# Kernel optimization log

Hardware: AMD Instinct MI355X
Metric: run time of the kernel (lower is better)

The kernel has to match this reference:

```python
import jax, jax.numpy as jnp
import numpy as np

B, C, H, W = 16, 512, 48, 48


def setup_inputs() -> dict:
    key = jax.random.key(0)
    k1, k2 = jax.random.split(key)
    rgb = jax.random.normal(k1, (B, C, H, W), dtype=jnp.float32)
    depth = jax.random.normal(k2, (B, C, H, W), dtype=jnp.float32)
    return {"rgb": rgb, "depth": depth}


def reference(rgb, depth):
    b, c, h, w = rgb.shape
    hw = h * w
    q = rgb.reshape(b, c, hw)              # [B, C, HW]
    k = depth.reshape(b, c, hw)            # [B, C, HW]
    # channel-affinity: energy[b, i, j] = <rgb_chan_i, depth_chan_j>
    energy = jnp.einsum('bcn,bdn->bcd', q, k)   # [B, C, C]
    cl_index = jnp.argmax(energy, axis=2)       # [B, C] best-matching depth channel per rgb channel
    # gather matched depth channels and fuse
    gathered = depth[jnp.arange(b)[:, None], cl_index]  # [B, C, H, W]
    return rgb + gathered
```

## Files before the change

kernel.cpp:

```cpp
#include <hip/hip_runtime.h>
#include <stdint.h>

#define BATCH 16
#define CH    512
#define HW    2304

typedef _Float16 half8  __attribute__((ext_vector_type(8)));
typedef float    f32x16 __attribute__((ext_vector_type(16)));

#define MFMA16 __builtin_amdgcn_mfma_f32_32x32x16_f16

#define DELTA 3.5f

#define ENERGY_ELEMS ((size_t)BATCH * CH * CH)
#define KSP     4
#define WS_NEED (KSP * ENERGY_ELEMS * 4)

#define LGKM_BARRIER() do { \
    asm volatile("s_waitcnt lgkmcnt(0)" ::: "memory"); \
    __builtin_amdgcn_s_barrier(); \
    __builtin_amdgcn_sched_barrier(0); \
} while (0)

__device__ __forceinline__ uint32_t f32_sortable(float f) {
    uint32_t u = __float_as_uint(f);
    return (u & 0x80000000u) ? ~u : (u | 0x80000000u);
}

__device__ __forceinline__ int swzs(int r, int s) {
    return r * 128 + ((s ^ ((r >> 1) & 7)) << 4);
}

__device__ __forceinline__ half8 cvt8h(const float4& v0, const float4& v1) {
    half8 h;
    h[0] = (_Float16)v0.x; h[1] = (_Float16)v0.y;
    h[2] = (_Float16)v0.z; h[3] = (_Float16)v0.w;
    h[4] = (_Float16)v1.x; h[5] = (_Float16)v1.y;
    h[6] = (_Float16)v1.z; h[7] = (_Float16)v1.w;
    return h;
}

#define BK3   64
#define KRANGE (HW / KSP)
#define NST   (KRANGE / BK3)
#define A3_OFF 0
#define B3_OFF 32768
#define BUF3_SZ 65536

__device__ __forceinline__ void load_tile3(const float* aT, const float* bT,
                                           float4 (&av)[8], float4 (&bv)[8]) {
    #pragma unroll
    for (int i = 0; i < 8; ++i) av[i] = *(const float4*)(aT + 4 * i);
    #pragma unroll
    for (int i = 0; i < 8; ++i) bv[i] = *(const float4*)(bT + 4 * i);
}

__device__ __forceinline__ void stage_tile3(char* dst,
                                            const float4 (&av)[8], const float4 (&bv)[8],
                                            int arow, int ah) {
    #pragma unroll
    for (int j = 0; j < 4; ++j)
        *(half8*)(dst + A3_OFF + swzs(arow, 4 * ah + j)) = cvt8h(av[2 * j], av[2 * j + 1]);
    #pragma unroll
    for (int j = 0; j < 4; ++j)
        *(half8*)(dst + B3_OFF + swzs(arow, 4 * ah + j)) = cvt8h(bv[2 * j], bv[2 * j + 1]);
}

__device__ __forceinline__ void compute_tile3(const char* buf, int rA0, int rB0, int hf,
                                              f32x16 (&acc)[2][4]) {
    __builtin_amdgcn_s_setprio(1);
    #pragma unroll
    for (int kc = 0; kc < 4; ++kc) {
        const int s0 = 2 * kc + hf;
        half8 a0 = *(const half8*)(buf + A3_OFF + swzs(rA0,      s0));
        half8 a1 = *(const half8*)(buf + A3_OFF + swzs(rA0 + 32, s0));
        half8 b0 = *(const half8*)(buf + B3_OFF + swzs(rB0,      s0));
        half8 b1 = *(const half8*)(buf + B3_OFF + swzs(rB0 + 32, s0));
        half8 b2 = *(const half8*)(buf + B3_OFF + swzs(rB0 + 64, s0));
        half8 b3 = *(const half8*)(buf + B3_OFF + swzs(rB0 + 96, s0));
        acc[0][0] = MFMA16(a0, b0, acc[0][0], 0, 0, 0);
        acc[0][1] = MFMA16(a0, b1, acc[0][1], 0, 0, 0);
        acc[0][2] = MFMA16(a0, b2, acc[0][2], 0, 0, 0);
        acc[0][3] = MFMA16(a0, b3, acc[0][3], 0, 0, 0);
        acc[1][0] = MFMA16(a1, b0, acc[1][0], 0, 0, 0);
        acc[1][1] = MFMA16(a1, b1, acc[1][1], 0, 0, 0);
        acc[1][2] = MFMA16(a1, b2, acc[1][2], 0, 0, 0);
        acc[1][3] = MFMA16(a1, b3, acc[1][3], 0, 0, 0);
    }
    __builtin_amdgcn_s_setprio(0);
}

__global__ __launch_bounds__(512, 2)
void screen3_kernel(const float* __restrict__ q,
                    const float* __restrict__ kmat,
                    float* __restrict__ epart)
{
    const int bid = blockIdx.x;
    const int nid = (bid & 7) * 32 + (bid >> 3);
    const int ks  = nid & 3;
    const int d0  = ((nid >> 2) & 1) * 256;
    const int c0  = ((nid >> 3) & 1) * 256;
    const int b   = nid >> 4;
    const int kbase = ks * KRANGE;

    const int tid  = threadIdx.x;
    const int lane = tid & 63;
    const int w    = tid >> 6;
    const int wm   = w >> 1;
    const int wn   = w & 1;

    __shared__ __align__(16) char sm[2 * BUF3_SZ];

    const int arow = tid >> 1, ah = tid & 1;
    const float* aG = q    + ((size_t)b * CH + c0 + arow) * HW + kbase + ah * 32;
    const float* bG = kmat + ((size_t)b * CH + d0 + arow) * HW + kbase + ah * 32;

    float4 av[8], bv[8];

    load_tile3(aG, bG, av, bv);
    stage_tile3(sm, av, bv, arow, ah);
    load_tile3(aG + BK3, bG + BK3, av, bv);
    LGKM_BARRIER();

    f32x16 acc[2][4] = {};
    const int rA0 = wm * 64 + (lane & 31);
    const int rB0 = wn * 128 + (lane & 31);
    const int hf  = lane >> 5;

    for (int t = 0; t < NST; ++t) {
        compute_tile3(sm + (size_t)(t & 1) * BUF3_SZ, rA0, rB0, hf, acc);
        if (t + 1 < NST) {
            stage_tile3(sm + (size_t)((t + 1) & 1) * BUF3_SZ, av, bv, arow, ah);
            LGKM_BARRIER();
            if (t + 2 < NST)
                load_tile3(aG + (t + 2) * BK3, bG + (t + 2) * BK3, av, bv);
        }
    }

    float* eb = epart + (size_t)ks * ENERGY_ELEMS
              + ((size_t)(b * CH + c0) * CH) + d0 + wn * 128 + (lane & 31);
    #pragma unroll
    for (int mi = 0; mi < 2; ++mi) {
        #pragma unroll
        for (int ni = 0; ni < 4; ++ni) {
            #pragma unroll
            for (int qr = 0; qr < 16; ++qr) {
                int rowl = wm * 64 + mi * 32 + (qr & 3) + 8 * (qr >> 2) + 4 * (lane >> 5);
                eb[(size_t)rowl * CH + ni * 32] = acc[mi][ni][qr];
            }
        }
    }
}

__global__ __launch_bounds__(256)
void rescore_gather_kernel(const float* __restrict__ rgb,
                           const float* __restrict__ depth,
                           const float* __restrict__ energy,
                           int np,
                           float* __restrict__ out)
{
    const int row = blockIdx.x;
    const int b   = row >> 9;
    const int tid = threadIdx.x;

    __shared__ float sred[4];
    __shared__ float sM;
    __shared__ int   scnt;
    __shared__ int   slist[CH];
    __shared__ unsigned long long sbest;

    const float* erow = energy + (size_t)row * CH;
    float e0 = 0.0f, e1 = 0.0f;
    for (int p = 0; p < np; ++p) {
        e0 += erow[(size_t)p * ENERGY_ELEMS + tid];
        e1 += erow[(size_t)p * ENERGY_ELEMS + tid + 256];
    }

    float m = fmaxf(e0, e1);
    #pragma unroll
    for (int off = 1; off < 64; off <<= 1) m = fmaxf(m, __shfl_xor(m, off, 64));
    if ((tid & 63) == 0) sred[tid >> 6] = m;
    __syncthreads();
    if (tid == 0) {
        sM = fmaxf(fmaxf(sred[0], sred[1]), fmaxf(sred[2], sred[3]));
        scnt = 0; sbest = 0ull;
    }
    __syncthreads();
    const float thr = sM - DELTA;
    if (e0 >= thr) { int i = atomicAdd(&scnt, 1); slist[i] = tid; }
    if (e1 >= thr) { int i = atomicAdd(&scnt, 1); slist[i] = tid + 256; }
    __syncthreads();
    const int cnt = scnt;

    const float4* q4 = (const float4*)(rgb + (size_t)row * HW);
    for (int i = 0; i < cnt; ++i) {
        const int d = slist[i];
        const float4* k4 = (const float4*)(depth + ((size_t)(b * CH + d)) * HW);
        float s = 0.0f;
        for (int j = tid; j < HW / 4; j += 256) {
            float4 a = q4[j], bb = k4[j];
            s += a.x * bb.x + a.y * bb.y + a.z * bb.z + a.w * bb.w;
        }
        #pragma unroll
        for (int off = 1; off < 64; off <<= 1) s += __shfl_xor(s, off, 64);
        if ((tid & 63) == 0) sred[tid >> 6] = s;
        __syncthreads();
        if (tid == 0) {
            float tot = sred[0] + sred[1] + sred[2] + sred[3];
            unsigned long long p =
                ((unsigned long long)f32_sortable(tot) << 32) |
                (uint32_t)(~(uint32_t)d);
            if (p > sbest) sbest = p;
        }
        __syncthreads();
    }

    const int widx = (int)(~(uint32_t)(sbest & 0xFFFFFFFFull));
    const float4* w4 = (const float4*)(depth + ((size_t)(b * CH + widx)) * HW);
    float4* o4 = (float4*)(out + (size_t)row * HW);
    for (int j = tid; j < HW / 4; j += 256) {
        float4 a = q4[j], dd = w4[j];
        o4[j] = make_float4(a.x + dd.x, a.y + dd.y, a.z + dd.z, a.w + dd.w);
    }
}

#define BKs   64
#define NKTs  (HW / BKs)
#define AHs_OFF 0
#define BHs_OFF 16384
#define BUFs_SZ 32768

__device__ __forceinline__ void load_tile_s(const float* aG, const float* bG, int k0,
                                            float4 (&av)[4], float4 (&bv)[4]) {
    av[0] = *(const float4*)(aG + k0 + 0);
    av[1] = *(const float4*)(aG + k0 + 4);
    av[2] = *(const float4*)(aG + k0 + 8);
    av[3] = *(const float4*)(aG + k0 + 12);
    bv[0] = *(const float4*)(bG + k0 + 0);
    bv[1] = *(const float4*)(bG + k0 + 4);
    bv[2] = *(const float4*)(bG + k0 + 8);
    bv[3] = *(const float4*)(bG + k0 + 12);
}

__device__ __forceinline__ void stage_tile_s(char* dst,
                                             const float4 (&av)[4], const float4 (&bv)[4],
                                             int row, int q) {
    *(half8*)(dst + AHs_OFF + swzs(row, 2 * q))     = cvt8h(av[0], av[1]);
    *(half8*)(dst + AHs_OFF + swzs(row, 2 * q + 1)) = cvt8h(av[2], av[3]);
    *(half8*)(dst + BHs_OFF + swzs(row, 2 * q))     = cvt8h(bv[0], bv[1]);
    *(half8*)(dst + BHs_OFF + swzs(row, 2 * q + 1)) = cvt8h(bv[2], bv[3]);
}

__device__ __forceinline__ void compute_tile_s(const char* buf, int rA0, int rB, int half,
                                               f32x16& acc0, f32x16& acc1) {
    __builtin_amdgcn_s_setprio(1);
    #pragma unroll
    for (int kc = 0; kc < 4; ++kc) {
        const int s0 = 2 * kc + half;
        half8 ah0 = *(const half8*)(buf + AHs_OFF + swzs(rA0,      s0));
        half8 ah1 = *(const half8*)(buf + AHs_OFF + swzs(rA0 + 32, s0));
        half8 bh  = *(const half8*)(buf + BHs_OFF + swzs(rB, s0));
        acc0 = MFMA16(ah0, bh, acc0, 0, 0, 0);
        acc1 = MFMA16(ah1, bh, acc1, 0, 0, 0);
    }
    __builtin_amdgcn_s_setprio(0);
}

__global__ __launch_bounds__(512, 1)
void screen_kernel(const float* __restrict__ q,
                   const float* __restrict__ kmat,
                   float* __restrict__ energy)
{
    const int bid = blockIdx.x;
    const int nid = (bid & 7) * 32 + (bid >> 3);
    const int d0  = (nid & 3) * 128;
    const int c0  = ((nid >> 2) & 3) * 128;
    const int b   = nid >> 4;

    const int tid  = threadIdx.x;
    const int lane = tid & 63;
    const int w    = tid >> 6;
    const int wm   = w >> 2;
    const int wn   = w & 3;

    __shared__ __align__(16) char sm[2 * BUFs_SZ];
    char* buf0 = sm;
    char* buf1 = sm + BUFs_SZ;

    const float* qb = q    + (size_t)b * CH * HW;
    const float* kb = kmat + (size_t)b * CH * HW;

    const int row = tid >> 2, sq = tid & 3;
    const float* aG = qb + (size_t)(c0 + row) * HW + sq * 16;
    const float* bG = kb + (size_t)(d0 + row) * HW + sq * 16;

    float4 av0[4], bv0[4], av1[4], bv1[4];

    load_tile_s(aG, bG, 0, av0, bv0);
    stage_tile_s(buf0, av0, bv0, row, sq);
    load_tile_s(aG, bG, BKs, av1, bv1);
    LGKM_BARRIER();

    f32x16 acc0 = {}, acc1 = {};
    const int rA0  = wm * 64 + (lane & 31);
    const int rB   = wn * 32 + (lane & 31);
    const int half = lane >> 5;

    for (int kt = 0; kt < NKTs; kt += 2) {
        if (kt + 2 < NKTs) load_tile_s(aG, bG, (kt + 2) * BKs, av0, bv0);
        stage_tile_s(buf1, av1, bv1, row, sq);
        compute_tile_s(buf0, rA0, rB, half, acc0, acc1);
        LGKM_BARRIER();
        if (kt + 3 < NKTs) load_tile_s(aG, bG, (kt + 3) * BKs, av1, bv1);
        if (kt + 2 < NKTs) stage_tile_s(buf0, av0, bv0, row, sq);
        compute_tile_s(buf1, rA0, rB, half, acc0, acc1);
        LGKM_BARRIER();
    }

    float* eb = energy + ((size_t)(b * CH + c0) * CH) + d0 + wn * 32 + (lane & 31);
    #pragma unroll
    for (int mi = 0; mi < 2; ++mi) {
        #pragma unroll
        for (int qr = 0; qr < 16; ++qr) {
            int rowl = wm * 64 + mi * 32 + (qr & 3) + 8 * (qr >> 2) + 4 * (lane >> 5);
            eb[(size_t)rowl * CH] = (mi == 0) ? acc0[qr] : acc1[qr];
        }
    }
}

extern "C" void kernel_launch(void* const* d_in, const int* in_sizes, int n_in,
                              void* d_out, int out_size, void* d_ws, size_t ws_size,
                              hipStream_t stream)
{
    const float* rgb   = (const float*)d_in[0];
    const float* depth = (const float*)d_in[1];
    float* out = (float*)d_out;
    float* energy = (float*)d_ws;

    if (ws_size >= WS_NEED) {
        screen3_kernel<<<256, 512, 0, stream>>>(rgb, depth, energy);
        rescore_gather_kernel<<<BATCH * CH, 256, 0, stream>>>(rgb, depth, energy, KSP, out);
    } else {
        screen_kernel<<<256, 512, 0, stream>>>(rgb, depth, energy);
        rescore_gather_kernel<<<BATCH * CH, 256, 0, stream>>>(rgb, depth, energy, 1, out);
    }
}
```

Measured before the change: 116.0 us.

## Restructure screen GEMM K-loop with BK=32 and two-deep register prefetch

```diff
diff --git a/kernel.cpp b/kernel.cpp
--- a/kernel.cpp
+++ b/kernel.cpp
@@ -25,6 +25,10 @@
 __device__ __forceinline__ uint32_t f32_sortable(float f) {
     uint32_t u = __float_as_uint(f);
     return (u & 0x80000000u) ? ~u : (u | 0x80000000u);
+}
+
+__device__ __forceinline__ int swzf(int r, int cb) {
+    return r * 64 + (cb ^ (((r >> 1) & 3) << 4));
 }
 
 __device__ __forceinline__ int swzs(int r, int s) {
@@ -40,44 +44,46 @@
     return h;
 }
 
-#define BK3   64
+#define BK3    32
 #define KRANGE (HW / KSP)
-#define NST   (KRANGE / BK3)
+#define NST    (KRANGE / BK3)
 #define A3_OFF 0
-#define B3_OFF 32768
-#define BUF3_SZ 65536
-
-__device__ __forceinline__ void load_tile3(const float* aT, const float* bT,
-                                           float4 (&av)[8], float4 (&bv)[8]) {
-    #pragma unroll
-    for (int i = 0; i < 8; ++i) av[i] = *(const float4*)(aT + 4 * i);
-    #pragma unroll
-    for (int i = 0; i < 8; ++i) bv[i] = *(const float4*)(bT + 4 * i);
+#define B3_OFF 16384
+#define BUF3_SZ 32768
+
+__device__ __forceinline__ void load_tile3(const float* aT, const float* bT, int k0,
+                                           float4 (&av)[4], float4 (&bv)[4]) {
+    av[0] = *(const float4*)(aT + k0 + 0);
+    av[1] = *(const float4*)(aT + k0 + 4);
+    av[2] = *(const float4*)(aT + k0 + 8);
+    av[3] = *(const float4*)(aT + k0 + 12);
+    bv[0] = *(const float4*)(bT + k0 + 0);
+    bv[1] = *(const float4*)(bT + k0 + 4);
+    bv[2] = *(const float4*)(bT + k0 + 8);
+    bv[3] = *(const float4*)(bT + k0 + 12);
 }
 
 __device__ __forceinline__ void stage_tile3(char* dst,
-                                            const float4 (&av)[8], const float4 (&bv)[8],
+                                            const float4 (&av)[4], const float4 (&bv)[4],
                                             int arow, int ah) {
-    #pragma unroll
-    for (int j = 0; j < 4; ++j)
-        *(half8*)(dst + A3_OFF + swzs(arow, 4 * ah + j)) = cvt8h(av[2 * j], av[2 * j + 1]);
-    #pragma unroll
-    for (int j = 0; j < 4; ++j)
-        *(half8*)(dst + B3_OFF + swzs(arow, 4 * ah + j)) = cvt8h(bv[2 * j], bv[2 * j + 1]);
-}
-
-__device__ __forceinline__ void compute_tile3(const char* buf, int rA0, int rB0, int hf,
+    *(half8*)(dst + A3_OFF + swzf(arow, 32 * ah))      = cvt8h(av[0], av[1]);
+    *(half8*)(dst + A3_OFF + swzf(arow, 32 * ah + 16)) = cvt8h(av[2], av[3]);
+    *(half8*)(dst + B3_OFF + swzf(arow, 32 * ah))      = cvt8h(bv[0], bv[1]);
+    *(half8*)(dst + B3_OFF + swzf(arow, 32 * ah + 16)) = cvt8h(bv[2], bv[3]);
+}
+
+__device__ __forceinline__ void compute_tile3(const char* buf, int rA0, int rB0, int hb,
                                               f32x16 (&acc)[2][4]) {
     __builtin_amdgcn_s_setprio(1);
     #pragma unroll
-    for (int kc = 0; kc < 4; ++kc) {
-        const int s0 = 2 * kc + hf;
-        half8 a0 = *(const half8*)(buf + A3_OFF + swzs(rA0,      s0));
-        half8 a1 = *(const half8*)(buf + A3_OFF + swzs(rA0 + 32, s0));
-        half8 b0 = *(const half8*)(buf + B3_OFF + swzs(rB0,      s0));
-        half8 b1 = *(const half8*)(buf + B3_OFF + swzs(rB0 + 32, s0));
-        half8 b2 = *(const half8*)(buf + B3_OFF + swzs(rB0 + 64, s0));
-        half8 b3 = *(const half8*)(buf + B3_OFF + swzs(rB0 + 96, s0));
+    for (int kc = 0; kc < 2; ++kc) {
+        const int cb = kc * 32 + hb;
+        half8 a0 = *(const half8*)(buf + A3_OFF + swzf(rA0,      cb));
+        half8 a1 = *(const half8*)(buf + A3_OFF + swzf(rA0 + 32, cb));
+        half8 b0 = *(const half8*)(buf + B3_OFF + swzf(rB0,      cb));
+        half8 b1 = *(const half8*)(buf + B3_OFF + swzf(rB0 + 32, cb));
+        half8 b2 = *(const half8*)(buf + B3_OFF + swzf(rB0 + 64, cb));
+        half8 b3 = *(const half8*)(buf + B3_OFF + swzf(rB0 + 96, cb));
         acc[0][0] = MFMA16(a0, b0, acc[0][0], 0, 0, 0);
         acc[0][1] = MFMA16(a0, b1, acc[0][1], 0, 0, 0);
         acc[0][2] = MFMA16(a0, b2, acc[0][2], 0, 0, 0);
@@ -90,7 +96,7 @@
     __builtin_amdgcn_s_setprio(0);
 }
 
-__global__ __launch_bounds__(512, 2)
+__global__ __launch_bounds__(512, 1)
 void screen3_kernel(const float* __restrict__ q,
                     const float* __restrict__ kmat,
                     float* __restrict__ epart)
@@ -110,31 +116,34 @@
     const int wn   = w & 1;
 
     __shared__ __align__(16) char sm[2 * BUF3_SZ];
+    char* buf0 = sm;
+    char* buf1 = sm + BUF3_SZ;
 
     const int arow = tid >> 1, ah = tid & 1;
-    const float* aG = q    + ((size_t)b * CH + c0 + arow) * HW + kbase + ah * 32;
-    const float* bG = kmat + ((size_t)b * CH + d0 + arow) * HW + kbase + ah * 32;
-
-    float4 av[8], bv[8];
-
-    load_tile3(aG, bG, av, bv);
-    stage_tile3(sm, av, bv, arow, ah);
-    load_tile3(aG + BK3, bG + BK3, av, bv);
+    const float* aG = q    + ((size_t)b * CH + c0 + arow) * HW + kbase + ah * 16;
+    const float* bG = kmat + ((size_t)b * CH + d0 + arow) * HW + kbase + ah * 16;
+
+    float4 av0[4], bv0[4], av1[4], bv1[4];
+
+    load_tile3(aG, bG, 0, av0, bv0);
+    stage_tile3(buf0, av0, bv0, arow, ah);
+    load_tile3(aG, bG, BK3, av1, bv1);
     LGKM_BARRIER();
 
     f32x16 acc[2][4] = {};
     const int rA0 = wm * 64 + (lane & 31);
     const int rB0 = wn * 128 + (lane & 31);
-    const int hf  = lane >> 5;
-
-    for (int t = 0; t < NST; ++t) {
-        compute_tile3(sm + (size_t)(t & 1) * BUF3_SZ, rA0, rB0, hf, acc);
-        if (t + 1 < NST) {
-            stage_tile3(sm + (size_t)((t + 1) & 1) * BUF3_SZ, av, bv, arow, ah);
-            LGKM_BARRIER();
-            if (t + 2 < NST)
-                load_tile3(aG + (t + 2) * BK3, bG + (t + 2) * BK3, av, bv);
-        }
+    const int hb  = (lane >> 5) * 16;
+
+    for (int kt = 0; kt < NST; kt += 2) {
+        if (kt + 2 < NST) load_tile3(aG, bG, (kt + 2) * BK3, av0, bv0);
+        stage_tile3(buf1, av1, bv1, arow, ah);
+        compute_tile3(buf0, rA0, rB0, hb, acc);
+        LGKM_BARRIER();
+        if (kt + 3 < NST) load_tile3(aG, bG, (kt + 3) * BK3, av1, bv1);
+        if (kt + 2 < NST) stage_tile3(buf0, av0, bv0, arow, ah);
+        compute_tile3(buf1, rA0, rB0, hb, acc);
+        LGKM_BARRIER();
     }
 
     float* eb = epart + (size_t)ks * ENERGY_ELEMS
```

After: 111.1 us. 4.3% less time.
